# Performance work log

Hardware: AMD Instinct MI355X
Metric: run time of the kernel (lower is better)

The kernel has to match this reference:

```python
import jax, jax.numpy as jnp
import numpy as np

DIM = 128
HEADS = 8
HEAD_DIM = DIM // HEADS
PE_DIM = 48
TEMP = 10000.0
WIN = 2
NUM_VALUES = WIN * WIN
SCALE = HEAD_DIM ** -0.5
TWO_PI = 2.0 * np.pi
EPS = 1e-6


def _interleave_sincos(p):
    # p [..., nf] -> interleaved sin(even)/cos(odd), matching torch stack+flatten
    s = jnp.sin(p[..., 0::2])
    c = jnp.cos(p[..., 1::2])
    return jnp.stack((s, c), axis=-1).reshape(p.shape)


def _dim_t(num_pos_feats):
    i = np.arange(num_pos_feats)
    return jnp.asarray(TEMP ** (2.0 * (i // 2) / num_pos_feats), dtype=jnp.float32)


def window_position_bias():
    nf = PE_DIM // 2
    ye = jnp.arange(WIN, dtype=jnp.float32)  # cumsum(ones)-1 along h
    xe = jnp.arange(WIN, dtype=jnp.float32)
    ye = ye / (ye[-1] + EPS) * TWO_PI
    xe = xe / (xe[-1] + EPS) * TWO_PI
    dt = _dim_t(nf)
    pos_y = ye[:, None, None] / dt
    pos_x = xe[None, :, None] / dt
    pos_y = jnp.broadcast_to(pos_y, (WIN, WIN, nf))
    pos_x = jnp.broadcast_to(pos_x, (WIN, WIN, nf))
    pe = jnp.concatenate((_interleave_sincos(pos_y), _interleave_sincos(pos_x)), axis=-1)
    return pe.reshape(NUM_VALUES, PE_DIM)


def points_position_encoding(points):
    # points [n, hw, 2] fractional offsets -> [n, hw, PE_DIM]
    nf = PE_DIM // 2
    ye = points[..., 0] / (WIN + EPS) * TWO_PI
    xe = points[..., 1] / (WIN + EPS) * TWO_PI
    dt = _dim_t(nf)
    pos_y = _interleave_sincos(ye[..., None] / dt)
    pos_x = _interleave_sincos(xe[..., None] / dt)
    return jnp.concatenate((pos_y, pos_x), axis=-1)


def setup_inputs() -> dict:
    key = jax.random.key(0)
    ks = jax.random.split(key, 12)
    n, c, h, w = 2, 48, 192, 192
    y = jax.random.normal(ks[0], (n, c, h, w), jnp.float32)
    x = jax.random.normal(ks[1], (n, c, h, w), jnp.float32)
    conv_w = jax.random.normal(ks[2], (1, 2 * PE_DIM, 3, 3), jnp.float32) * 0.05
    conv_b = jnp.zeros((1,), jnp.float32)
    q_w = jax.random.normal(ks[3], (PE_DIM, DIM), jnp.float32) * (PE_DIM ** -0.5)
    q_b = jnp.zeros((DIM,), jnp.float32)
    k_w = jax.random.normal(ks[4], (PE_DIM, DIM), jnp.float32) * (PE_DIM ** -0.5)
    k_b = jnp.zeros((DIM,), jnp.float32)
    v_w = jax.random.normal(ks[5], (PE_DIM, DIM), jnp.float32) * (PE_DIM ** -0.5)
    v_b = jnp.zeros((DIM,), jnp.float32)
    return {"y": y, "x": x, "conv_w": conv_w, "conv_b": conv_b,
            "q_w": q_w, "q_b": q_b, "k_w": k_w, "k_b": k_b, "v_w": v_w, "v_b": v_b}


def reference(y, x, conv_w, conv_b, q_w, q_b, k_w, k_b, v_w, v_b):
    n, c, h, w = x.shape
    hw = h * w
    # per-pixel horizontal offset from both feature maps
    off = jax.lax.conv_general_dilated(
        jnp.concatenate([y, x], axis=1), conv_w, (1, 1), ((1, 1), (1, 1)),
        dimension_numbers=("NCHW", "OIHW", "NCHW")) + conv_b[None, :, None, None]
    off = jnp.transpose(off, (0, 2, 3, 1)) * (2.0 / w)  # [n,h,w,1]

    gh, gw = jnp.meshgrid(jnp.arange(h, dtype=x.dtype), jnp.arange(w, dtype=x.dtype), indexing="ij")
    # flow.flip(-1) puts the offset on the w coordinate only
    grid_wrp = jnp.stack(
        (jnp.broadcast_to(gh, (n, h, w)),
         gw[None] + off[..., 0]), axis=-1)                      # [n,h,w,2]
    flr = jnp.floor(grid_wrp)
    frac = (grid_wrp - flr).reshape(n, hw, 2)
    flr = flr.reshape(n, hw, 2)

    widx = jnp.array([[0, 0], [0, 1], [1, 0], [1, 1]], dtype=x.dtype)  # window_idx_offset
    g4 = (flr[:, :, None, :] + widx).reshape(n, hw * NUM_VALUES, 2)

    idx0 = jnp.clip(g4[..., 0], 0, h - 1).astype(jnp.int32)
    idx1 = jnp.clip(g4[..., 1], 0, w - 1).astype(jnp.int32)
    lin = idx1 + w * idx0                                      # [n, hw*4]
    wrp = jnp.take_along_axis(y.reshape(n, c, hw), lin[:, None, :], axis=2)  # [n,c,hw*4]
    wrp = jnp.transpose(wrp, (0, 2, 1))                        # [n, hw*4, c]

    # pe_dim // c == 1 tiling; add window position bias per pixel
    pb = window_position_bias()                                # [4, PE_DIM]
    wrp = (wrp.reshape(n, hw, NUM_VALUES, PE_DIM) + pb).reshape(n, hw * NUM_VALUES, PE_DIM)

    x_flat = jnp.transpose(x.reshape(n, c, hw), (0, 2, 1))     # [n, hw, c]
    x_in = x_flat + points_position_encoding(frac)

    nhw = n * hw
    q = (x_in @ q_w + q_b).reshape(nhw, HEADS, HEAD_DIM)
    k = (wrp @ k_w + k_b).reshape(nhw, NUM_VALUES, HEADS, HEAD_DIM)
    v = (wrp @ v_w + v_b).reshape(nhw, NUM_VALUES, HEADS, HEAD_DIM)

    attn = jnp.einsum("phd,pkhd->phk", q * SCALE, k)           # [nhw, heads, 4]
    attn = jax.nn.softmax(attn, axis=-1)
    out = jnp.einsum("phk,pkhd->phd", attn, v).reshape(nhw, DIM)
    return jnp.transpose(out.reshape(n, h, w, DIM), (0, 3, 1, 2))
```

## Files before the change

### kernel.cpp

```cpp
#include <hip/hip_runtime.h>
#include <hip/hip_bf16.h>

#define HW_ 36864
#define W_ 192
#define H_ 192
#define NPIX_ 73728
#define TWO_PI_F 6.283185307179586f

typedef __attribute__((ext_vector_type(8))) short bfrag;
typedef __attribute__((ext_vector_type(4))) float f4;

__device__ __constant__ float DT_G[12] = {
    1.0f, 2.154434690031884f, 4.641588833612779f, 10.0f,
    21.54434690031884f, 46.41588833612779f, 100.0f, 215.4434690031884f,
    464.1588833612779f, 1000.0f, 2154.434690031884f, 4641.588833612779f};

__device__ __forceinline__ unsigned short f2bf(float f) {
    __hip_bfloat16 h = __float2bfloat16(f);
    unsigned short u;
    __builtin_memcpy(&u, &h, 2);
    return u;
}

__device__ __forceinline__ int a_idx(int tile, int m, int k) {
    return tile * 1024 + ((k >> 5) << 9) + (m << 3) + (((k >> 3) & 3) << 7) + (k & 7);
}

__device__ __forceinline__ int rsw(int r) { return ((r & 3) << 2) | (r >> 2); }

__device__ __forceinline__ float red16(float v) {
    int t;
    t = __builtin_amdgcn_update_dpp(0, __float_as_int(v), 0x128, 0xF, 0xF, true);
    v += __int_as_float(t);
    t = __builtin_amdgcn_update_dpp(0, __float_as_int(v), 0x124, 0xF, 0xF, true);
    v += __int_as_float(t);
    t = __builtin_amdgcn_update_dpp(0, __float_as_int(v), 0x122, 0xF, 0xF, true);
    v += __int_as_float(t);
    t = __builtin_amdgcn_update_dpp(0, __float_as_int(v), 0x121, 0xF, 0xF, true);
    v += __int_as_float(t);
    return v;
}

__global__ void prep_wfrag(const float* __restrict__ qw, const float* __restrict__ kw,
                           const float* __restrict__ vw, unsigned short* __restrict__ wsb) {
    int idx = blockIdx.x * 256 + threadIdx.x;
    if (idx >= 24576) return;
    int j = idx & 7;
    int lane = (idx >> 3) & 63;
    int ks = (idx >> 9) & 1;
    int h = (idx >> 10) & 7;
    int mat = idx >> 13;
    const float* w = (mat == 0) ? qw : (mat == 1) ? kw : vw;
    int k = ks * 32 + ((lane >> 4) << 3) + j;
    int n = (h << 4) + (lane & 15);
    float f = (k < 48) ? w[k * 128 + n] : 0.0f;
    wsb[idx] = f2bf(f);
}

struct __align__(16) Smem {
    unsigned short A[10 * 1024];
    float outt[128 * 33];
    float pbl[192];
    float offs[32];
    float part[8][32];
};

__global__ __launch_bounds__(512, 4) void fused_kernel(
    const float* __restrict__ y, const float* __restrict__ x,
    const float* __restrict__ cw, const float* __restrict__ cb,
    const float* __restrict__ qb, const float* __restrict__ kb,
    const float* __restrict__ vb, const unsigned short* __restrict__ wsb,
    float* __restrict__ out) {
    __shared__ Smem sm;
    int tid = threadIdx.x;
    int bid = blockIdx.x;
    int b = (bid & 7) * 288 + (bid >> 3);
    int pix0 = b * 32;
    int n = pix0 / HW_;
    int rem0 = pix0 - n * HW_;
    int row0 = rem0 / W_;
    int col0 = rem0 - row0 * W_;

    float xv8[8];
    if (tid < 256) {
        int p = tid & 31, q = tid >> 5;
        int col = col0 + p;
        float m_lf = (col > 0) ? 1.f : 0.f, m_rt = (col < W_ - 1) ? 1.f : 0.f;
        float m_up = (row0 > 0) ? 1.f : 0.f, m_dn = (row0 < H_ - 1) ? 1.f : 0.f;
        int c_lf = col - (col > 0 ? 1 : 0);
        int c_rt = col + (col < W_ - 1 ? 1 : 0);
        int r_up = row0 - (row0 > 0 ? 1 : 0);
        int r_dn = row0 + (row0 < H_ - 1 ? 1 : 0);
        float k0 = m_up * m_lf, k1 = m_up, k2 = m_up * m_rt;
        float k3 = m_lf, k5 = m_rt;
        float k6 = m_dn * m_lf, k7 = m_dn, k8 = m_dn * m_rt;
        int icbase = (q >> 1) * 24 + (q & 1) * 12;
        float acc = 0.f;
#pragma unroll
        for (int g2 = 0; g2 < 4; ++g2) {
            float buf[27];
#pragma unroll
            for (int cc = 0; cc < 3; ++cc) {
                int ic = icbase + g2 * 3 + cc;
                const float* src = (ic < 48) ? y : x;
                int c = (ic < 48) ? ic : ic - 48;
                const float* b0p = src + (size_t)(n * 48 + c) * HW_;
                const float* pu = b0p + (size_t)r_up * W_;
                const float* pm = b0p + (size_t)row0 * W_;
                const float* pd = b0p + (size_t)r_dn * W_;
                buf[cc * 9 + 0] = pu[c_lf];
                buf[cc * 9 + 1] = pu[col];
                buf[cc * 9 + 2] = pu[c_rt];
                buf[cc * 9 + 3] = pm[c_lf];
                buf[cc * 9 + 4] = pm[col];
                buf[cc * 9 + 5] = pm[c_rt];
                buf[cc * 9 + 6] = pd[c_lf];
                buf[cc * 9 + 7] = pd[col];
                buf[cc * 9 + 8] = pd[c_rt];
            }
#pragma unroll
            for (int cc = 0; cc < 3; ++cc) {
                int ic = icbase + g2 * 3 + cc;
                const float* wp = cw + ic * 9;
                acc += buf[cc * 9 + 0] * (wp[0] * k0);
                acc += buf[cc * 9 + 1] * (wp[1] * k1);
                acc += buf[cc * 9 + 2] * (wp[2] * k2);
                acc += buf[cc * 9 + 3] * (wp[3] * k3);
                acc += buf[cc * 9 + 4] * wp[4];
                acc += buf[cc * 9 + 5] * (wp[5] * k5);
                acc += buf[cc * 9 + 6] * (wp[6] * k6);
                acc += buf[cc * 9 + 7] * (wp[7] * k7);
                acc += buf[cc * 9 + 8] * (wp[8] * k8);
            }
        }
        sm.part[q][p] = acc;
    } else {
        int e = tid - 256, p = e & 31, oct = e >> 5;
        if (oct < 6) {
            const float* xb = x + (size_t)(n * 48 + oct * 8) * HW_ + rem0 + p;
#pragma unroll
            for (int j = 0; j < 8; ++j) xv8[j] = xb[(size_t)j * HW_];
        }
        if (e < 192) {
            int v = e / 48, c = e - (e / 48) * 48;
            int iy = v >> 1, ix = v & 1;
            int cc = (c < 24) ? c : c - 24;
            int sel = (c < 24) ? iy : ix;
            float ee = sel ? (TWO_PI_F / (1.0f + 1e-6f)) : 0.0f;
            float arg = ee / DT_G[cc >> 1];
            sm.pbl[v * 48 + c] = (cc & 1) ? __cosf(arg) : __sinf(arg);
        }
    }
    __syncthreads();
    if (tid < 32) {
        float a = sm.part[0][tid];
#pragma unroll
        for (int s = 1; s < 8; ++s) a += sm.part[s][tid];
        sm.offs[tid] = (a + cb[0]) * (2.0f / (float)W_);
    }
    __syncthreads();

    float yv[16];
    int r_w = tid & 127, oct_w = tid >> 7, t_w = 0, m_w = 0, v_w = 0;
    bool do_wrp = tid < 384;
    if (do_wrp) {
        int p = r_w >> 2;
        v_w = r_w & 3;
        float o = sm.offs[p];
        float gx = (float)(col0 + p) + o;
        float fx = floorf(gx);
        int dy = v_w >> 1, dx = v_w & 1;
        int rr = (int)fminf(fmaxf((float)(row0 + dy), 0.0f), 191.0f);
        int ccx = (int)fminf(fmaxf(fx + (float)dx, 0.0f), 191.0f);
        const float* yb = y + (size_t)(n * 48) * HW_ + (size_t)rr * W_ + ccx;
#pragma unroll
        for (int j = 0; j < 8; ++j) yv[j] = yb[(size_t)(oct_w * 8 + j) * HW_];
#pragma unroll
        for (int j = 0; j < 8; ++j) yv[8 + j] = yb[(size_t)((oct_w + 3) * 8 + j) * HW_];
        t_w = 2 + (r_w >> 4);
        m_w = r_w & 15;
    }
    if (tid >= 256) {
        int e = tid - 256, p = e & 31, oct = e >> 5;
        bfrag w0;
        if (oct < 6) {
            float o = sm.offs[p];
            float gx = (float)(col0 + p) + o;
            float fr = gx - floorf(gx);
            float t1 = fr / (2.0f + 1e-6f);
#pragma unroll
            for (int j = 0; j < 8; ++j) {
                float pe;
                if (oct < 3) {
                    pe = (j & 1) ? 1.0f : 0.0f;
                } else {
                    int cc = oct * 8 + j - 24;
                    float arg = (t1 * TWO_PI_F) / DT_G[cc >> 1];
                    pe = (cc & 1) ? __cosf(arg) : __sinf(arg);
                }
                w0[j] = (short)f2bf(xv8[j] + pe);
            }
        } else {
#pragma unroll
            for (int j = 0; j < 8; ++j) w0[j] = 0;
        }
        *(bfrag*)&sm.A[a_idx(p >> 4, rsw(p & 15), oct * 8)] = w0;
    } else {
        int r = tid & 127, o2 = 6 + (tid >> 7);
        bfrag z;
#pragma unroll
        for (int j = 0; j < 8; ++j) z[j] = 0;
        *(bfrag*)&sm.A[a_idx(2 + (r >> 4), r & 15, o2 * 8)] = z;
    }
    if (do_wrp) {
        bfrag w0, w1;
#pragma unroll
        for (int j = 0; j < 8; ++j)
            w0[j] = (short)f2bf(yv[j] + sm.pbl[v_w * 48 + oct_w * 8 + j]);
#pragma unroll
        for (int j = 0; j < 8; ++j)
            w1[j] = (short)f2bf(yv[8 + j] + sm.pbl[v_w * 48 + (oct_w + 3) * 8 + j]);
        *(bfrag*)&sm.A[a_idx(t_w, m_w, oct_w * 8)] = w0;
        *(bfrag*)&sm.A[a_idx(t_w, m_w, (oct_w + 3) * 8)] = w1;
    }
    __syncthreads();

    int lane = tid & 63, h = tid >> 6;
    int lq = lane & 15, lg = lane >> 4;
    float qbv = qb[(h << 4) + lq];
    float kbv = kb[(h << 4) + lq];
    float vbv = vb[(h << 4) + lq];

    const int hb = (h << 1) * 64 + lane;
    bfrag qB0 = *(const bfrag*)&wsb[(0 * 1024 + hb) * 8];
    bfrag qB1 = *(const bfrag*)&wsb[(0 * 1024 + hb + 64) * 8];
    bfrag kB0 = *(const bfrag*)&wsb[(1 * 1024 + hb) * 8];
    bfrag kB1 = *(const bfrag*)&wsb[(1 * 1024 + hb + 64) * 8];
    bfrag vB0 = *(const bfrag*)&wsb[(2 * 1024 + hb) * 8];
    bfrag vB1 = *(const bfrag*)&wsb[(2 * 1024 + hb + 64) * 8];

    f4 qacc[2];
#pragma unroll
    for (int t = 0; t < 2; ++t) {
        bfrag a0 = *(const bfrag*)&sm.A[t * 1024 + lane * 8];
        bfrag a1 = *(const bfrag*)&sm.A[t * 1024 + 512 + lane * 8];
        f4 a = {qbv, qbv, qbv, qbv};
        a = __builtin_amdgcn_mfma_f32_16x16x32_bf16(a0, qB0, a, 0, 0, 0);
        a = __builtin_amdgcn_mfma_f32_16x16x32_bf16(a1, qB1, a, 0, 0, 0);
        qacc[t] = a;
    }

#pragma unroll
    for (int m = 0; m < 8; ++m) {
        bfrag a0 = *(const bfrag*)&sm.A[(2 + m) * 1024 + lane * 8];
        bfrag a1 = *(const bfrag*)&sm.A[(2 + m) * 1024 + 512 + lane * 8];
        f4 ka = {kbv, kbv, kbv, kbv};
        ka = __builtin_amdgcn_mfma_f32_16x16x32_bf16(a0, kB0, ka, 0, 0, 0);
        ka = __builtin_amdgcn_mfma_f32_16x16x32_bf16(a1, kB1, ka, 0, 0, 0);
        f4 va = {vbv, vbv, vbv, vbv};
        va = __builtin_amdgcn_mfma_f32_16x16x32_bf16(a0, vB0, va, 0, 0, 0);
        va = __builtin_amdgcn_mfma_f32_16x16x32_bf16(a1, vB1, va, 0, 0, 0);

        f4 qa = qacc[m >> 2];
        float qv = ((m & 3) == 0) ? qa.x : ((m & 3) == 1) ? qa.y
                 : ((m & 3) == 2) ? qa.z : qa.w;
        qv *= 0.25f;

        float s0 = qv * ka.x, s1 = qv * ka.y, s2 = qv * ka.z, s3 = qv * ka.w;
        s0 = red16(s0);
        s1 = red16(s1);
        s2 = red16(s2);
        s3 = red16(s3);
        float mx = fmaxf(fmaxf(s0, s1), fmaxf(s2, s3));
        float e0 = __expf(s0 - mx), e1 = __expf(s1 - mx);
        float e2 = __expf(s2 - mx), e3 = __expf(s3 - mx);
        float rden = 1.0f / (e0 + e1 + e2 + e3);
        float o = (e0 * va.x + e1 * va.y + e2 * va.z + e3 * va.w) * rden;
        sm.outt[((h << 4) + lq) * 33 + (m << 2) + lg] = o;
    }
    __syncthreads();

    {
        int ch = tid >> 2, q4 = tid & 3;
        const float* sp = &sm.outt[ch * 33 + q4 * 8];
        float4* dst = (float4*)(out + (size_t)(n * 128 + ch) * HW_ + rem0 + q4 * 8);
        dst[0] = make_float4(sp[0], sp[1], sp[2], sp[3]);
        dst[1] = make_float4(sp[4], sp[5], sp[6], sp[7]);
    }
}

extern "C" void kernel_launch(void* const* d_in, const int* in_sizes, int n_in,
                              void* d_out, int out_size, void* d_ws, size_t ws_size,
                              hipStream_t stream) {
    unsigned short* wsb = (unsigned short*)d_ws;
    hipLaunchKernelGGL(prep_wfrag, dim3(96), dim3(256), 0, stream,
                       (const float*)d_in[4], (const float*)d_in[6],
                       (const float*)d_in[8], wsb);
    hipLaunchKernelGGL(fused_kernel, dim3(NPIX_ / 32), dim3(512), 0, stream,
                       (const float*)d_in[0], (const float*)d_in[1],
                       (const float*)d_in[2], (const float*)d_in[3],
                       (const float*)d_in[5], (const float*)d_in[7],
                       (const float*)d_in[9], wsb,
                       (float*)d_out);
}
```

Before: 135.6 us.

## Transpose MFMA operand roles so head dims sit in rows and pixels in columns

Swaps the MFMA A/B operands so weights become the A operand and pixel/window rows the B operand, and reorders the K/V tile rows so each group of four lanes holds the four window values of one pixel. Softmax and the weighted sum then run with two-step DPP reductions over those four lanes instead of 16-lane reductions per score. Q is now recomputed inside the loop, once per tile, rather than precomputed. Launch bounds are raised to 8 for more occupancy, which risks register spilling.

```diff
diff --git a/kernel.cpp b/kernel.cpp
--- a/kernel.cpp
+++ b/kernel.cpp
@@ -26,18 +26,18 @@
     return tile * 1024 + ((k >> 5) << 9) + (m << 3) + (((k >> 3) & 3) << 7) + (k & 7);
 }
 
-__device__ __forceinline__ int rsw(int r) { return ((r & 3) << 2) | (r >> 2); }
-
-__device__ __forceinline__ float red16(float v) {
-    int t;
+__device__ __forceinline__ float vgrp_sum(float v) {
+    int t = __builtin_amdgcn_update_dpp(0, __float_as_int(v), 0x124, 0xF, 0xF, true);
+    v += __int_as_float(t);
     t = __builtin_amdgcn_update_dpp(0, __float_as_int(v), 0x128, 0xF, 0xF, true);
     v += __int_as_float(t);
-    t = __builtin_amdgcn_update_dpp(0, __float_as_int(v), 0x124, 0xF, 0xF, true);
-    v += __int_as_float(t);
-    t = __builtin_amdgcn_update_dpp(0, __float_as_int(v), 0x122, 0xF, 0xF, true);
-    v += __int_as_float(t);
-    t = __builtin_amdgcn_update_dpp(0, __float_as_int(v), 0x121, 0xF, 0xF, true);
-    v += __int_as_float(t);
+    return v;
+}
+__device__ __forceinline__ float vgrp_max(float v) {
+    int t = __builtin_amdgcn_update_dpp(0, __float_as_int(v), 0x124, 0xF, 0xF, true);
+    v = fmaxf(v, __int_as_float(t));
+    t = __builtin_amdgcn_update_dpp(0, __float_as_int(v), 0x128, 0xF, 0xF, true);
+    v = fmaxf(v, __int_as_float(t));
     return v;
 }
 
@@ -65,7 +65,7 @@
     float part[8][32];
 };
 
-__global__ __launch_bounds__(512, 4) void fused_kernel(
+__global__ __launch_bounds__(512, 8) void fused_kernel(
     const float* __restrict__ y, const float* __restrict__ x,
     const float* __restrict__ cw, const float* __restrict__ cb,
     const float* __restrict__ qb, const float* __restrict__ kb,
@@ -161,7 +161,7 @@
     __syncthreads();
 
     float yv[16];
-    int r_w = tid & 127, oct_w = tid >> 7, t_w = 0, m_w = 0, v_w = 0;
+    int r_w = tid & 127, oct_w = tid >> 7, t_w = 0, rt_w = 0, v_w = 0;
     bool do_wrp = tid < 384;
     if (do_wrp) {
         int p = r_w >> 2;
@@ -177,8 +177,8 @@
         for (int j = 0; j < 8; ++j) yv[j] = yb[(size_t)(oct_w * 8 + j) * HW_];
 #pragma unroll
         for (int j = 0; j < 8; ++j) yv[8 + j] = yb[(size_t)((oct_w + 3) * 8 + j) * HW_];
-        t_w = 2 + (r_w >> 4);
-        m_w = r_w & 15;
+        t_w = 2 + (p >> 2);
+        rt_w = (v_w << 2) | (p & 3);
     }
     if (tid >= 256) {
         int e = tid - 256, p = e & 31, oct = e >> 5;
@@ -204,7 +204,7 @@
 #pragma unroll
             for (int j = 0; j < 8; ++j) w0[j] = 0;
         }
-        *(bfrag*)&sm.A[a_idx(p >> 4, rsw(p & 15), oct * 8)] = w0;
+        *(bfrag*)&sm.A[a_idx(p >> 4, p & 15, oct * 8)] = w0;
     } else {
         int r = tid & 127, o2 = 6 + (tid >> 7);
         bfrag z;
@@ -220,63 +220,63 @@
 #pragma unroll
         for (int j = 0; j < 8; ++j)
             w1[j] = (short)f2bf(yv[8 + j] + sm.pbl[v_w * 48 + (oct_w + 3) * 8 + j]);
-        *(bfrag*)&sm.A[a_idx(t_w, m_w, oct_w * 8)] = w0;
-        *(bfrag*)&sm.A[a_idx(t_w, m_w, (oct_w + 3) * 8)] = w1;
+        *(bfrag*)&sm.A[a_idx(t_w, rt_w, oct_w * 8)] = w0;
+        *(bfrag*)&sm.A[a_idx(t_w, rt_w, (oct_w + 3) * 8)] = w1;
     }
     __syncthreads();
 
     int lane = tid & 63, h = tid >> 6;
     int lq = lane & 15, lg = lane >> 4;
-    float qbv = qb[(h << 4) + lq];
-    float kbv = kb[(h << 4) + lq];
-    float vbv = vb[(h << 4) + lq];
+    f4 qbv = *(const f4*)&qb[(h << 4) + (lg << 2)];
+    f4 kbv = *(const f4*)&kb[(h << 4) + (lg << 2)];
+    f4 vbv = *(const f4*)&vb[(h << 4) + (lg << 2)];
 
     const int hb = (h << 1) * 64 + lane;
-    bfrag qB0 = *(const bfrag*)&wsb[(0 * 1024 + hb) * 8];
-    bfrag qB1 = *(const bfrag*)&wsb[(0 * 1024 + hb + 64) * 8];
-    bfrag kB0 = *(const bfrag*)&wsb[(1 * 1024 + hb) * 8];
-    bfrag kB1 = *(const bfrag*)&wsb[(1 * 1024 + hb + 64) * 8];
-    bfrag vB0 = *(const bfrag*)&wsb[(2 * 1024 + hb) * 8];
-    bfrag vB1 = *(const bfrag*)&wsb[(2 * 1024 + hb + 64) * 8];
-
-    f4 qacc[2];
-#pragma unroll
-    for (int t = 0; t < 2; ++t) {
-        bfrag a0 = *(const bfrag*)&sm.A[t * 1024 + lane * 8];
-        bfrag a1 = *(const bfrag*)&sm.A[t * 1024 + 512 + lane * 8];
-        f4 a = {qbv, qbv, qbv, qbv};
-        a = __builtin_amdgcn_mfma_f32_16x16x32_bf16(a0, qB0, a, 0, 0, 0);
-        a = __builtin_amdgcn_mfma_f32_16x16x32_bf16(a1, qB1, a, 0, 0, 0);
-        qacc[t] = a;
-    }
+    bfrag qW0 = *(const bfrag*)&wsb[(0 * 1024 + hb) * 8];
+    bfrag qW1 = *(const bfrag*)&wsb[(0 * 1024 + hb + 64) * 8];
+    bfrag kW0 = *(const bfrag*)&wsb[(1 * 1024 + hb) * 8];
+    bfrag kW1 = *(const bfrag*)&wsb[(1 * 1024 + hb + 64) * 8];
+    bfrag vW0 = *(const bfrag*)&wsb[(2 * 1024 + hb) * 8];
+    bfrag vW1 = *(const bfrag*)&wsb[(2 * 1024 + hb + 64) * 8];
+
+    int vg = lq >> 2, px = lq & 3;
+    int obase = ((h << 4) + (lg << 2) + vg) * 33 + px;
 
 #pragma unroll
     for (int m = 0; m < 8; ++m) {
-        bfrag a0 = *(const bfrag*)&sm.A[(2 + m) * 1024 + lane * 8];
-        bfrag a1 = *(const bfrag*)&sm.A[(2 + m) * 1024 + 512 + lane * 8];
-        f4 ka = {kbv, kbv, kbv, kbv};
-        ka = __builtin_amdgcn_mfma_f32_16x16x32_bf16(a0, kB0, ka, 0, 0, 0);
-        ka = __builtin_amdgcn_mfma_f32_16x16x32_bf16(a1, kB1, ka, 0, 0, 0);
-        f4 va = {vbv, vbv, vbv, vbv};
-        va = __builtin_amdgcn_mfma_f32_16x16x32_bf16(a0, vB0, va, 0, 0, 0);
-        va = __builtin_amdgcn_mfma_f32_16x16x32_bf16(a1, vB1, va, 0, 0, 0);
-
-        f4 qa = qacc[m >> 2];
-        float qv = ((m & 3) == 0) ? qa.x : ((m & 3) == 1) ? qa.y
-                 : ((m & 3) == 2) ? qa.z : qa.w;
-        qv *= 0.25f;
-
-        float s0 = qv * ka.x, s1 = qv * ka.y, s2 = qv * ka.z, s3 = qv * ka.w;
-        s0 = red16(s0);
-        s1 = red16(s1);
-        s2 = red16(s2);
-        s3 = red16(s3);
-        float mx = fmaxf(fmaxf(s0, s1), fmaxf(s2, s3));
-        float e0 = __expf(s0 - mx), e1 = __expf(s1 - mx);
-        float e2 = __expf(s2 - mx), e3 = __expf(s3 - mx);
-        float rden = 1.0f / (e0 + e1 + e2 + e3);
-        float o = (e0 * va.x + e1 * va.y + e2 * va.z + e3 * va.w) * rden;
-        sm.outt[((h << 4) + lq) * 33 + (m << 2) + lg] = o;
+        bfrag b0 = *(const bfrag*)&sm.A[(2 + m) * 1024 + lane * 8];
+        bfrag b1 = *(const bfrag*)&sm.A[(2 + m) * 1024 + 512 + lane * 8];
+        int qcol = ((m & 3) << 2) | px;
+        int qoff = ((m >> 2) << 10) + ((lane >> 4) << 7) + (qcol << 3);
+        bfrag x0 = *(const bfrag*)&sm.A[qoff];
+        bfrag x1 = *(const bfrag*)&sm.A[qoff + 512];
+
+        f4 ka = kbv;
+        ka = __builtin_amdgcn_mfma_f32_16x16x32_bf16(kW0, b0, ka, 0, 0, 0);
+        ka = __builtin_amdgcn_mfma_f32_16x16x32_bf16(kW1, b1, ka, 0, 0, 0);
+        f4 va = vbv;
+        va = __builtin_amdgcn_mfma_f32_16x16x32_bf16(vW0, b0, va, 0, 0, 0);
+        va = __builtin_amdgcn_mfma_f32_16x16x32_bf16(vW1, b1, va, 0, 0, 0);
+        f4 qa = qbv;
+        qa = __builtin_amdgcn_mfma_f32_16x16x32_bf16(qW0, x0, qa, 0, 0, 0);
+        qa = __builtin_amdgcn_mfma_f32_16x16x32_bf16(qW1, x1, qa, 0, 0, 0);
+
+        float sp = qa.x * ka.x + qa.y * ka.y + qa.z * ka.z + qa.w * ka.w;
+        sp += __shfl_xor(sp, 16);
+        sp += __shfl_xor(sp, 32);
+        float s = sp * 0.25f;
+
+        float mx = vgrp_max(s);
+        float e = __expf(s - mx);
+        float den = vgrp_sum(e);
+        float w = e * (1.0f / den);
+
+        float o0 = vgrp_sum(w * va.x);
+        float o1 = vgrp_sum(w * va.y);
+        float o2 = vgrp_sum(w * va.z);
+        float o3 = vgrp_sum(w * va.w);
+        float ov = (vg == 0) ? o0 : (vg == 1) ? o1 : (vg == 2) ? o2 : o3;
+        sm.outt[obase + (m << 2)] = ov;
     }
     __syncthreads();
 
```

After: 146.7 us. +8.2%, slower.
